# Kernel optimization log

Measured on AMD Instinct MI355X. Metric: run time of the kernel, lower is better.

## Reference

```python
import jax, jax.numpy as jnp
import numpy as np

B, C, H, W, NH = 8, 256, 32, 32, 4  # batch, channels, height, width, heads


def groupnorm(x, w, b, eps=1e-5):
    # GroupNorm with 1 group: normalize over (C,H,W) per sample
    mu = x.mean(axis=(1, 2, 3), keepdims=True)
    var = x.var(axis=(1, 2, 3), keepdims=True)
    xn = (x - mu) * jax.lax.rsqrt(var + eps)
    return xn * w[None, :, None, None] + b[None, :, None, None]


def setup_inputs() -> dict:
    key = jax.random.key(0)
    ks = jax.random.split(key, 6)
    C4 = 4 * C
    s = lambda k, shape, scale: jax.random.normal(k, shape, jnp.float32) * scale
    return {
        "x": jax.random.normal(ks[0], (B, C, H, W), jnp.float32),
        "qkv_w": s(ks[1], (3 * C, C), 0.05),   # 1x1 conv, no bias
        "uh_w": s(ks[2], (C, C), 0.05),
        "uh_b": jnp.zeros((C,), jnp.float32),
        "n1_w": jnp.ones((C,), jnp.float32),
        "n1_b": jnp.zeros((C,), jnp.float32),
        "n2_w": jnp.ones((C,), jnp.float32),
        "n2_b": jnp.zeros((C,), jnp.float32),
        "f1_w": s(ks[3], (C4, C), 0.05),
        "f1_b": jnp.zeros((C4,), jnp.float32),
        "f2_w": s(ks[4], (C, C4), 0.05),
        "f2_b": jnp.zeros((C,), jnp.float32),
        # torch inits these to 0; use nonzero values so both branches contribute
        "gamma_attn": jnp.array(0.5, jnp.float32),
        "gamma_ffn": jnp.array(0.5, jnp.float32),
    }


def reference(x, qkv_w, uh_w, uh_b, n1_w, n1_b, n2_w, n2_b,
              f1_w, f1_b, f2_w, f2_b, gamma_attn, gamma_ffn):
    Bx, Cx, Hx, Wx = x.shape
    N = Hx * Wx
    dk = Cx // NH
    # --- attention branch (eval mode: DropPath is identity) ---
    xn = groupnorm(x, n1_w, n1_b).reshape(Bx, Cx, N)
    qkv = jnp.einsum('oc,bcn->bon', qkv_w, xn)          # 1x1 conv == channel matmul
    q, k, v = [t.reshape(Bx, NH, dk, N) for t in jnp.split(qkv, 3, axis=1)]
    scores = jnp.einsum('bhdi,bhdj->bhij', q, k) / np.float32(np.sqrt(dk))
    attn = jax.nn.softmax(scores, axis=-1)               # [B,H,N,N]
    out = jnp.einsum('bhij,bhdj->bhdi', attn, v).reshape(Bx, Cx, N)
    uh = jnp.einsum('oc,bcn->bon', uh_w, out) + uh_b[None, :, None]
    x2 = x + gamma_attn * uh.reshape(Bx, Cx, Hx, Wx)
    # --- FFN branch ---
    h = groupnorm(x2, n2_w, n2_b).reshape(Bx, Cx, N)
    h = jax.nn.silu(jnp.einsum('oc,bcn->bon', f1_w, h) + f1_b[None, :, None])
    h = jnp.einsum('oc,bcn->bon', f2_w, h) + f2_b[None, :, None]
    return x2 + gamma_ffn * h.reshape(Bx, Cx, Hx, Wx)
```

## Files before the change

### kernel.cpp

```cpp
#include <hip/hip_runtime.h>
#include <math.h>

#define Bsz 8
#define Cch 256
#define Nsp 1024
#define NHd 4
#define QS  0.18033688011112042f

using bf16x8  = __attribute__((ext_vector_type(8))) short;
using f32x4   = __attribute__((ext_vector_type(4))) float;
using ushort8 = __attribute__((ext_vector_type(8))) unsigned short;
#define MFMA(a,b,c) __builtin_amdgcn_mfma_f32_16x16x32_bf16(a,b,c,0,0,0)

__device__ inline unsigned short f2bf(float f) {
    unsigned int u = __float_as_uint(f);
    u = u + 0x7fffu + ((u >> 16) & 1u);
    return (unsigned short)(u >> 16);
}
__device__ inline float bf2f(unsigned short u) {
    return __uint_as_float((unsigned int)u << 16);
}
__device__ inline unsigned int cvtpk(float lo, float hi) {
    unsigned int r;
    asm("v_cvt_pk_bf16_f32 %0, %1, %2" : "=v"(r) : "v"(lo), "v"(hi));
    return r;
}

__global__ __launch_bounds__(256) void wconv_gn(const float* __restrict__ a, const float* __restrict__ b,
                                                const float* __restrict__ c, const float* __restrict__ d,
                                                unsigned short* __restrict__ o,
                                                const float* __restrict__ x,
                                                float* __restrict__ part) {
    if (blockIdx.x < 3072) {
        size_t i = (size_t)blockIdx.x * 256 + threadIdx.x;
        float v;
        if (i < 196608) v = a[i];
        else if (i < 262144) v = b[i - 196608];
        else if (i < 524288) v = c[i - 262144];
        else v = d[i - 524288];
        o[i] = f2bf(v);
        return;
    }
    int blk = blockIdx.x - 3072;
    int bb = blk >> 6;
    const float* xb = x + (size_t)bb * (Cch * Nsp) + (size_t)(blk & 63) * 4096;
    int t = threadIdx.x;
    float s = 0.f, s2 = 0.f;
    for (int i = t; i < 4096; i += 256) { float v = xb[i]; s += v; s2 += v * v; }
    __shared__ float sh[256], sh2[256];
    sh[t] = s; sh2[t] = s2; __syncthreads();
    for (int off = 128; off; off >>= 1) {
        if (t < off) { sh[t] += sh[t + off]; sh2[t] += sh2[t + off]; }
        __syncthreads();
    }
    if (t == 0) { part[blk * 2] = sh[0]; part[blk * 2 + 1] = sh2[0]; }
}

template<int K, int KL, int NFRAG>
__global__ __launch_bounds__(256, 4) void gemm_lds(
        const unsigned short* __restrict__ W,
        const unsigned short* __restrict__ Xcl,
        int epi, int act, int xmode,
        unsigned short* __restrict__ ocl, int Ocl, int ocol0,
        unsigned short* __restrict__ orm,
        float* __restrict__ pf, const float* __restrict__ res,
        unsigned short* __restrict__ x2cl,
        const float* __restrict__ gamma, const float* __restrict__ bias,
        float* __restrict__ part,
        const float* __restrict__ gnpart,
        const float* __restrict__ gnw, const float* __restrict__ gnb) {
    static_assert(KL == 256 && K == 256, "single-round K only");
    constexpr int NTILE = NFRAG * 16;
    constexpr int CPR = KL / 8;
    constexpr int TOTCH = NTILE * CPR;
    int b = blockIdx.z, nb = blockIdx.x, ob = blockIdx.y;
    int t = threadIdx.x, w = t >> 6, l = t & 63, lg = l >> 4, lm = l & 15;
    __shared__ unsigned short Xs[NTILE * KL];
    __shared__ float sgn[2];
    const unsigned short* Xb = Xcl + ((size_t)b * Nsp + nb * NTILE) * K;
    int o_base = ob * 256 + w * 64;
    const unsigned short* Wp = W + (size_t)(o_base + lm) * K + 8 * lg;
    int m8 = lm & 7;

    bf16x8 wA0, wA1, wA2, wA3, wB0, wB1, wB2, wB3, wC0, wC1, wC2, wC3;
    #define WL(d0, d1, d2, d3, ks_) do {                                   \
        d0 = *(const bf16x8*)(Wp + (size_t)(0)      + (ks_) * 32);         \
        d1 = *(const bf16x8*)(Wp + (size_t)16 * K   + (ks_) * 32);         \
        d2 = *(const bf16x8*)(Wp + (size_t)32 * K   + (ks_) * 32);         \
        d3 = *(const bf16x8*)(Wp + (size_t)48 * K   + (ks_) * 32);         \
    } while (0)
    WL(wA0, wA1, wA2, wA3, 0);
    WL(wB0, wB1, wB2, wB3, 1);

    if (xmode == 0) {
        #pragma unroll
        for (int i = 0; i < TOTCH / 256; i++) {
            int c = i * 256 + t;
            int n = c / CPR, s = c % CPR;
            int gc = s ^ (n & 7);
            *(bf16x8*)&Xs[c * 8] = *(const bf16x8*)(Xb + (size_t)n * K + gc * 8);
        }
    } else if (xmode == 1) {
        if (t < 64) {
            float s = gnpart[(b * 64 + t) * 2], s2 = gnpart[(b * 64 + t) * 2 + 1];
            for (int m = 1; m < 64; m <<= 1) { s += __shfl_xor(s, m); s2 += __shfl_xor(s2, m); }
            if (t == 0) {
                float inv_n = 1.f / (Cch * Nsp);
                float mu = s * inv_n;
                float var = s2 * inv_n - mu * mu;
                sgn[0] = mu; sgn[1] = rsqrtf(var + 1e-5f);
            }
        }
        __syncthreads();
        float mu = sgn[0], rs = sgn[1];
        #pragma unroll
        for (int i = 0; i < TOTCH / 256; i++) {
            int c = i * 256 + t;
            int n = c / CPR, s = c % CPR;
            int gc = s ^ (n & 7);
            ushort8 xv = *(const ushort8*)(Xb + (size_t)n * K + gc * 8);
            f32x4 w0 = *(const f32x4*)(gnw + gc * 8);
            f32x4 w1 = *(const f32x4*)(gnw + gc * 8 + 4);
            f32x4 b0 = *(const f32x4*)(gnb + gc * 8);
            f32x4 b1 = *(const f32x4*)(gnb + gc * 8 + 4);
            ushort8 rr;
            #pragma unroll
            for (int j = 0; j < 4; j++) {
                rr[j]     = f2bf((bf2f(xv[j])     - mu) * rs * w0[j] + b0[j]);
                rr[4 + j] = f2bf((bf2f(xv[4 + j]) - mu) * rs * w1[j] + b1[j]);
            }
            *(ushort8*)&Xs[c * 8] = rr;
        }
    } else if (xmode == 2) {
        const size_t SPO = (size_t)Bsz * Nsp * Cch;
        #pragma unroll
        for (int i = 0; i < TOTCH / 256; i++) {
            int c = i * 256 + t;
            int n = c / CPR, s = c % CPR;
            int gc = s ^ (n & 7);
            const unsigned short* p0 = Xb + (size_t)n * K + gc * 8;
            int h = gc >> 3;
            int gn = nb * NTILE + n;
            float a0[8] = {};
            float lsum = 0.f;
            #pragma unroll
            for (int sp = 0; sp < 4; sp++) {
                ushort8 ov = *(const ushort8*)(p0 + (size_t)sp * SPO);
                #pragma unroll
                for (int j = 0; j < 8; j++) a0[j] += bf2f(ov[j]);
                lsum += gnpart[(((size_t)sp * Bsz + b) * NHd + h) * Nsp + gn];
            }
            float inv = 1.f / lsum;
            ushort8 rr;
            #pragma unroll
            for (int j = 0; j < 8; j++) rr[j] = f2bf(a0[j] * inv);
            *(ushort8*)&Xs[c * 8] = rr;
        }
    } else {
        if (t < 64) {
            float s = gnpart[(b * 64 + t) * 2], s2 = gnpart[(b * 64 + t) * 2 + 1];
            for (int m = 1; m < 64; m <<= 1) { s += __shfl_xor(s, m); s2 += __shfl_xor(s2, m); }
            if (t == 0) {
                float inv_n = 1.f / (Cch * Nsp);
                float mu = s * inv_n;
                float var = s2 * inv_n - mu * mu;
                sgn[0] = mu; sgn[1] = rsqrtf(var + 1e-5f);
            }
        }
        __syncthreads();
        float mu = sgn[0], rs = sgn[1];
        int n = t & 31;
        #pragma unroll
        for (int i = 0; i < 4; i++) {
            int G = i * 8 + (t >> 5);
            const float* xr = res + ((size_t)b * Cch + G * 8) * Nsp + (size_t)nb * NTILE + n;
            ushort8 rr;
            #pragma unroll
            for (int j = 0; j < 8; j++) {
                float val = xr[(size_t)j * Nsp];
                rr[j] = f2bf((val - mu) * rs * gnw[G * 8 + j] + gnb[G * 8 + j]);
            }
            int slot = G ^ (n & 7);
            *(ushort8*)&Xs[(n * 32 + slot) * 8] = rr;
        }
    }
    __syncthreads();

    f32x4 acc[4][NFRAG] = {};
    #define KS(w0_, w1_, w2_, w3_, ks_) do {                               \
        _Pragma("unroll")                                                  \
        for (int nf = 0; nf < NFRAG; nf++) {                               \
            int slot = ((ks_) * 4 + lg) ^ m8;                              \
            bf16x8 xf = *(const bf16x8*)&Xs[((nf * 16 + lm) * CPR + slot) * 8]; \
            acc[0][nf] = MFMA(w0_, xf, acc[0][nf]);                        \
            acc[1][nf] = MFMA(w1_, xf, acc[1][nf]);                        \
            acc[2][nf] = MFMA(w2_, xf, acc[2][nf]);                        \
            acc[3][nf] = MFMA(w3_, xf, acc[3][nf]);                        \
        }                                                                  \
    } while (0)
    WL(wC0, wC1, wC2, wC3, 2); KS(wA0, wA1, wA2, wA3, 0);
    WL(wA0, wA1, wA2, wA3, 3); KS(wB0, wB1, wB2, wB3, 1);
    WL(wB0, wB1, wB2, wB3, 4); KS(wC0, wC1, wC2, wC3, 2);
    WL(wC0, wC1, wC2, wC3, 5); KS(wA0, wA1, wA2, wA3, 3);
    WL(wA0, wA1, wA2, wA3, 6); KS(wB0, wB1, wB2, wB3, 4);
    WL(wB0, wB1, wB2, wB3, 7); KS(wC0, wC1, wC2, wC3, 5);
    KS(wA0, wA1, wA2, wA3, 6);
    KS(wB0, wB1, wB2, wB3, 7);
    #undef WL
    #undef KS

    if (epi == 0) {
        if (act == 3 && o_base >= 512) {
            #pragma unroll
            for (int nf = 0; nf < NFRAG; nf++) {
                int n = nb * NTILE + nf * 16 + lm;
                #pragma unroll
                for (int q = 0; q < 4; q++)
                    #pragma unroll
                    for (int r = 0; r < 4; r++) {
                        int o = o_base + q * 16 + 4 * lg + r - 512;
                        orm[((size_t)b * Cch + o) * Nsp + n] = f2bf(acc[q][nf][r]);
                    }
            }
        } else {
            float sc = (act == 3 && o_base < 256) ? QS : 1.f;
            #pragma unroll
            for (int nf = 0; nf < NFRAG; nf++) {
                int n = nb * NTILE + nf * 16 + lm;
                unsigned short* dst = ocl + ((size_t)b * Nsp + n) * Ocl + ocol0 + o_base + 4 * lg;
                #pragma unroll
                for (int q = 0; q < 4; q++) {
                    unsigned long long pk = 0;
                    #pragma unroll
                    for (int r = 0; r < 4; r++) {
                        int o = o_base + q * 16 + 4 * lg + r;
                        float v = acc[q][nf][r];
                        if (bias) v += bias[o];
                        if (act == 1) v = v / (1.f + __expf(-v));
                        else v *= sc;
                        pk |= (unsigned long long)f2bf(v) << (16 * r);
                    }
                    *(unsigned long long*)(dst + q * 16) = pk;
                }
            }
        }
    } else {
        float g = gamma[0];
        float ps = 0.f, ps2 = 0.f;
        #pragma unroll
        for (int nf = 0; nf < NFRAG; nf++) {
            int n = nb * NTILE + nf * 16 + lm;
            unsigned short* cdst = x2cl + ((size_t)b * Nsp + n) * Cch + o_base + 4 * lg;
            #pragma unroll
            for (int q = 0; q < 4; q++) {
                unsigned long long pk = 0;
                #pragma unroll
                for (int r = 0; r < 4; r++) {
                    int o = o_base + q * 16 + 4 * lg + r;
                    float v = acc[q][nf][r];
                    if (bias) v += bias[o];
                    size_t idx = ((size_t)b * Cch + o) * Nsp + n;
                    float ov = res[idx] + g * v;
                    pf[idx] = ov;
                    ps += ov; ps2 += ov * ov;
                    pk |= (unsigned long long)f2bf(ov) << (16 * r);
                }
                *(unsigned long long*)(cdst + q * 16) = pk;
            }
        }
        float* rsh  = (float*)&Xs[0];
        float* rsh2 = rsh + 256;
        __syncthreads();
        rsh[t] = ps; rsh2[t] = ps2; __syncthreads();
        for (int off = 128; off; off >>= 1) {
            if (t < off) { rsh[t] += rsh[t + off]; rsh2[t] += rsh2[t + off]; }
            __syncthreads();
        }
        if (t == 0) {
            int slot = b * gridDim.x + nb;
            part[slot * 2] = rsh[0]; part[slot * 2 + 1] = rsh2[0];
        }
    }
}

__global__ __launch_bounds__(512, 2) void ffn_fused(
        const unsigned short* __restrict__ Wf1,
        const unsigned short* __restrict__ Wf2,
        const unsigned short* __restrict__ x2cl,
        const float* __restrict__ gnpart,
        const float* __restrict__ gnw, const float* __restrict__ gnb,
        const float* __restrict__ f1b, const float* __restrict__ f2b,
        const float* __restrict__ gamma,
        const float* __restrict__ x2, float* __restrict__ out) {
    int b = blockIdx.z, nb = blockIdx.x;
    int t = threadIdx.x, w = t >> 6, l = t & 63, lg = l >> 4, lm = l & 15;
    int wq = w >> 2, wr = w & 3;
    __shared__ unsigned short Xs[32 * 256];
    __shared__ unsigned short H[4][32 * 256];
    __shared__ float sgn[2];
    const unsigned short* Xb = x2cl + ((size_t)b * Nsp + nb * 32) * 256;
    int m8 = lm & 7;

    bf16x8 wA0, wA1, wA2, wA3, wB0, wB1, wB2, wB3, wC0, wC1, wC2, wC3;
    const unsigned short* Wp;
    #define WL1(d0, d1, d2, d3, ks_) do {                                  \
        d0 = *(const bf16x8*)(Wp + (ks_) * 32);                            \
        d1 = *(const bf16x8*)(Wp + (size_t)16 * 256 + (ks_) * 32);         \
        d2 = *(const bf16x8*)(Wp + (size_t)32 * 256 + (ks_) * 32);         \
        d3 = *(const bf16x8*)(Wp + (size_t)48 * 256 + (ks_) * 32);         \
    } while (0)

    if (t < 64) {
        float s = gnpart[(b * 64 + t) * 2], s2 = gnpart[(b * 64 + t) * 2 + 1];
        for (int m = 1; m < 64; m <<= 1) { s += __shfl_xor(s, m); s2 += __shfl_xor(s2, m); }
        if (t == 0) {
            float inv_n = 1.f / (Cch * Nsp);
            float mu = s * inv_n;
            float var = s2 * inv_n - mu * mu;
            sgn[0] = mu; sgn[1] = rsqrtf(var + 1e-5f);
        }
    }
    Wp = Wf1 + (size_t)(wq * 256 + wr * 64 + lm) * 256 + 8 * lg;
    WL1(wA0, wA1, wA2, wA3, 0);
    WL1(wB0, wB1, wB2, wB3, 1);
    __syncthreads();
    {
        float mu = sgn[0], rs = sgn[1];
        #pragma unroll
        for (int i = 0; i < 2; i++) {
            int c = i * 512 + t;
            int n = c >> 5, s = c & 31;
            int gc = s ^ (n & 7);
            ushort8 xv = *(const ushort8*)(Xb + (size_t)n * 256 + gc * 8);
            f32x4 w0 = *(const f32x4*)(gnw + gc * 8);
            f32x4 w1 = *(const f32x4*)(gnw + gc * 8 + 4);
            f32x4 b0 = *(const f32x4*)(gnb + gc * 8);
            f32x4 b1 = *(const f32x4*)(gnb + gc * 8 + 4);
            ushort8 rr;
            #pragma unroll
            for (int j = 0; j < 4; j++) {
                rr[j]     = f2bf((bf2f(xv[j])     - mu) * rs * w0[j] + b0[j]);
                rr[4 + j] = f2bf((bf2f(xv[4 + j]) - mu) * rs * w1[j] + b1[j]);
            }
            *(ushort8*)&Xs[c * 8] = rr;
        }
    }
    __syncthreads();

    f32x4 acc[4][2];
    #define KS1(w0_, w1_, w2_, w3_, ks_) do {                              \
        _Pragma("unroll")                                                  \
        for (int nf = 0; nf < 2; nf++) {                                   \
            int slot = ((ks_) * 4 + lg) ^ m8;                              \
            bf16x8 xf = *(const bf16x8*)&Xs[((nf * 16 + lm) * 32 + slot) * 8]; \
            acc[0][nf] = MFMA(w0_, xf, acc[0][nf]);                        \
            acc[1][nf] = MFMA(w1_, xf, acc[1][nf]);                        \
            acc[2][nf] = MFMA(w2_, xf, acc[2][nf]);                        \
            acc[3][nf] = MFMA(w3_, xf, acc[3][nf]);                        \
        }                                                                  \
    } while (0)
    #define F1CHAIN() do {                                                 \
        WL1(wC0, wC1, wC2, wC3, 2); KS1(wA0, wA1, wA2, wA3, 0);            \
        WL1(wA0, wA1, wA2, wA3, 3); KS1(wB0, wB1, wB2, wB3, 1);            \
        WL1(wB0, wB1, wB2, wB3, 4); KS1(wC0, wC1, wC2, wC3, 2);            \
        WL1(wC0, wC1, wC2, wC3, 5); KS1(wA0, wA1, wA2, wA3, 3);            \
        WL1(wA0, wA1, wA2, wA3, 6); KS1(wB0, wB1, wB2, wB3, 4);            \
        WL1(wB0, wB1, wB2, wB3, 7); KS1(wC0, wC1, wC2, wC3, 5);            \
        KS1(wA0, wA1, wA2, wA3, 6);                                        \
        KS1(wB0, wB1, wB2, wB3, 7);                                        \
    } while (0)
    #define F1EPI(p_) do {                                                 \
        int hb = (p_) * 2 + wq;                                            \
        _Pragma("unroll")                                                  \
        for (int nf = 0; nf < 2; nf++) {                                   \
            int n = nf * 16 + lm;                                          \
            _Pragma("unroll")                                              \
            for (int q = 0; q < 4; q++) {                                  \
                unsigned long long pk = 0;                                 \
                _Pragma("unroll")                                          \
                for (int r = 0; r < 4; r++) {                              \
                    int oin = wr * 64 + q * 16 + 4 * lg + r;               \
                    float v = acc[q][nf][r] + f1b[(p_) * 512 + wq * 256 + oin]; \
                    v = v / (1.f + __expf(-v));                            \
                    pk |= (unsigned long long)f2bf(v) << (16 * r);         \
                }                                                          \
                int G = wr * 8 + q * 2 + (lg >> 1);                        \
                int slot = G ^ (n & 7);                                    \
                *(unsigned long long*)&H[hb][(n * 32 + slot) * 8 + 4 * (lg & 1)] = pk; \
            }                                                              \
        }                                                                  \
    } while (0)

    #pragma unroll
    for (int q = 0; q < 4; q++)
        #pragma unroll
        for (int nf = 0; nf < 2; nf++) acc[q][nf] = (f32x4){0.f, 0.f, 0.f, 0.f};
    F1CHAIN();
    Wp = Wf1 + (size_t)(512 + wq * 256 + wr * 64 + lm) * 256 + 8 * lg;
    WL1(wA0, wA1, wA2, wA3, 0);
    WL1(wB0, wB1, wB2, wB3, 1);
    F1EPI(0);
    #pragma unroll
    for (int q = 0; q < 4; q++)
        #pragma unroll
        for (int nf = 0; nf < 2; nf++) acc[q][nf] = (f32x4){0.f, 0.f, 0.f, 0.f};
    F1CHAIN();
    #undef WL1
    #undef KS1
    #undef F1CHAIN

    const unsigned short* Wp2 = Wf2 + (size_t)(w * 32 + lm) * 1024 + 8 * lg;
    bf16x8 u0, u1, v0, v1, z0, z1;
    #define WL2(d0, d1, ks_) do {                                          \
        d0 = *(const bf16x8*)(Wp2 + (ks_) * 32);                           \
        d1 = *(const bf16x8*)(Wp2 + (size_t)16 * 1024 + (ks_) * 32);       \
    } while (0)
    WL2(u0, u1, 0);
    WL2(v0, v1, 1);
    F1EPI(1);
    #undef F1EPI
    __syncthreads();

    f32x4 ac2[2][2] = {};
    #define KS2(e0, e1, g_) do {                                           \
        int slot = (((g_) & 7) * 4 + lg) ^ m8;                             \
        const unsigned short* Hp = H[(g_) >> 3];                           \
        _Pragma("unroll")                                                  \
        for (int nf = 0; nf < 2; nf++) {                                   \
            bf16x8 xf = *(const bf16x8*)&Hp[((nf * 16 + lm) * 32 + slot) * 8]; \
            ac2[0][nf] = MFMA(e0, xf, ac2[0][nf]);                         \
            ac2[1][nf] = MFMA(e1, xf, ac2[1][nf]);                         \
        }                                                                  \
    } while (0)
    WL2(z0, z1, 2);  KS2(u0, u1, 0);
    WL2(u0, u1, 3);  KS2(v0, v1, 1);
    WL2(v0, v1, 4);  KS2(z0, z1, 2);
    WL2(z0, z1, 5);  KS2(u0, u1, 3);
    WL2(u0, u1, 6);  KS2(v0, v1, 4);
    WL2(v0, v1, 7);  KS2(z0, z1, 5);
    WL2(z0, z1, 8);  KS2(u0, u1, 6);
    WL2(u0, u1, 9);  KS2(v0, v1, 7);
    WL2(v0, v1, 10); KS2(z0, z1, 8);
    WL2(z0, z1, 11); KS2(u0, u1, 9);
    WL2(u0, u1, 12); KS2(v0, v1, 10);
    WL2(v0, v1, 13); KS2(z0, z1, 11);
    WL2(z0, z1, 14); KS2(u0, u1, 12);
    WL2(u0, u1, 15); KS2(v0, v1, 13);
    WL2(v0, v1, 16); KS2(z0, z1, 14);
    WL2(z0, z1, 17); KS2(u0, u1, 15);
    WL2(u0, u1, 18); KS2(v0, v1, 16);
    WL2(v0, v1, 19); KS2(z0, z1, 17);
    WL2(z0, z1, 20); KS2(u0, u1, 18);
    WL2(u0, u1, 21); KS2(v0, v1, 19);
    WL2(v0, v1, 22); KS2(z0, z1, 20);
    WL2(z0, z1, 23); KS2(u0, u1, 21);
    WL2(u0, u1, 24); KS2(v0, v1, 22);
    WL2(v0, v1, 25); KS2(z0, z1, 23);
    WL2(z0, z1, 26); KS2(u0, u1, 24);
    WL2(u0, u1, 27); KS2(v0, v1, 25);
    WL2(v0, v1, 28); KS2(z0, z1, 26);
    WL2(z0, z1, 29); KS2(u0, u1, 27);
    WL2(u0, u1, 30); KS2(v0, v1, 28);
    WL2(v0, v1, 31); KS2(z0, z1, 29);
    KS2(u0, u1, 30);
    KS2(v0, v1, 31);
    #undef WL2
    #undef KS2

    float gm = gamma[0];
    #pragma unroll
    for (int nf = 0; nf < 2; nf++) {
        int n = nb * 32 + nf * 16 + lm;
        #pragma unroll
        for (int ch = 0; ch < 2; ch++) {
            #pragma unroll
            for (int r = 0; r < 4; r++) {
                int o = w * 32 + ch * 16 + 4 * lg + r;
                size_t idx = ((size_t)b * Cch + o) * Nsp + n;
                out[idx] = x2[idx] + gm * (ac2[ch][nf][r] + f2b[o]);
            }
        }
    }
}

__global__ __launch_bounds__(256) void attn_mfma8(const unsigned short* __restrict__ qk,
                                                  const unsigned short* __restrict__ v,
                                                  unsigned short* __restrict__ Opart,
                                                  float* __restrict__ lpart) {
    int L = blockIdx.x;
    int xcd = L & 7, jj = L >> 3;
    int g = xcd * 4 + (jj >> 5);
    int m = jj & 31;
    int h = g & 3, b = g >> 2;
    int ib = m & 7, sp = m >> 3;
    int t = threadIdx.x, w = t >> 6, l = t & 63, lg = l >> 4, lm = l & 15;
    __shared__ unsigned short KVs[2][4096];
    __shared__ unsigned short P[4][2][32][36];
    int i0 = ib * 128 + w * 32;
    int j0 = sp * 256;
    const unsigned short* qb = qk + ((size_t)b * Nsp + i0 + lm) * 512 + h * 64 + 8 * lg;
    bf16x8 qf00 = *(const bf16x8*)(qb);
    bf16x8 qf01 = *(const bf16x8*)(qb + 32);
    bf16x8 qf10 = *(const bf16x8*)(qb + 16 * 512);
    bf16x8 qf11 = *(const bf16x8*)(qb + 16 * 512 + 32);

    const unsigned short *gs0, *gs1;
    int lo0, lo1;
    size_t gstep;
    if (t < 128) {
        int c = 2 * t;
        int r = c >> 3, s = c & 7, swr = r & 7;
        const unsigned short* rowp = qk + ((size_t)b * Nsp + j0 + r) * 512 + 256 + h * 64;
        gs0 = rowp + ((s ^ swr) * 8);
        gs1 = rowp + (((s + 1) ^ swr) * 8);
        lo0 = c * 8; lo1 = lo0 + 8;
        gstep = (size_t)32 * 512;
    } else {
        int c = 2 * (t - 128);
        int d = c >> 2, s = c & 3, swd = d & 3;
        const unsigned short* rowp = v + ((size_t)b * Cch + h * 64 + d) * Nsp + j0;
        gs0 = rowp + ((s ^ swd) * 8);
        gs1 = rowp + (((s + 1) ^ swd) * 8);
        lo0 = 2048 + c * 8; lo1 = lo0 + 8;
        gstep = 32;
    }
    int cA = (lg ^ (lm & 7)) * 8;
    int cB = ((4 + lg) ^ (lm & 7)) * 8;
    int cV = (lg ^ (lm & 3)) * 8;

    f32x4 O00 = {}, O01 = {}, O02 = {}, O03 = {};
    f32x4 O10 = {}, O11 = {}, O12 = {}, O13 = {};
    float ls0 = 0.f, ls1 = 0.f;
    bf16x8 sg0, sg1;

    #define ISSUE(tile) do { sg0 = *(const bf16x8*)(gs0 + (size_t)(tile) * gstep); \
                             sg1 = *(const bf16x8*)(gs1 + (size_t)(tile) * gstep); } while (0)
    #define WRITE(bu) do { *(bf16x8*)&KVs[bu][lo0] = sg0; \
                           *(bf16x8*)&KVs[bu][lo1] = sg1; } while (0)
    #define QKC8(bu, pb) do {                                                     \
        const unsigned short* Ka = KVs[bu] + lm * 64;                             \
        const unsigned short* Kc = KVs[bu] + (16 + lm) * 64;                      \
        bf16x8 k00 = *(const bf16x8*)(Ka + cA);                                   \
        bf16x8 k01 = *(const bf16x8*)(Ka + cB);                                   \
        bf16x8 k10 = *(const bf16x8*)(Kc + cA);                                   \
        bf16x8 k11 = *(const bf16x8*)(Kc + cB);                                   \
        f32x4 s00 = {}, s01 = {}, s10 = {}, s11 = {};                             \
        s00 = MFMA(k00, qf00, s00); s00 = MFMA(k01, qf01, s00);                   \
        s01 = MFMA(k00, qf10, s01); s01 = MFMA(k01, qf11, s01);                   \
        s10 = MFMA(k10, qf00, s10); s10 = MFMA(k11, qf01, s10);                   \
        s11 = MFMA(k10, qf10, s11); s11 = MFMA(k11, qf11, s11);                   \
        float p0, p1, p2, p3; uint2 pk;                                           \
        p0 = exp2f(s00[0]); p1 = exp2f(s00[1]); p2 = exp2f(s00[2]); p3 = exp2f(s00[3]); \
        ls0 += (p0 + p1) + (p2 + p3);                                             \
        pk.x = cvtpk(p0, p1); pk.y = cvtpk(p2, p3);                               \
        *(uint2*)&P[w][pb][lm][4 * lg] = pk;                                      \
        p0 = exp2f(s01[0]); p1 = exp2f(s01[1]); p2 = exp2f(s01[2]); p3 = exp2f(s01[3]); \
        ls1 += (p0 + p1) + (p2 + p3);                                             \
        pk.x = cvtpk(p0, p1); pk.y = cvtpk(p2, p3);                               \
        *(uint2*)&P[w][pb][16 + lm][4 * lg] = pk;                                 \
        p0 = exp2f(s10[0]); p1 = exp2f(s10[1]); p2 = exp2f(s10[2]); p3 = exp2f(s10[3]); \
        ls0 += (p0 + p1) + (p2 + p3);                                             \
        pk.x = cvtpk(p0, p1); pk.y = cvtpk(p2, p3);                               \
        *(uint2*)&P[w][pb][lm][16 + 4 * lg] = pk;                                 \
        p0 = exp2f(s11[0]); p1 = exp2f(s11[1]); p2 = exp2f(s11[2]); p3 = exp2f(s11[3]); \
        ls1 += (p0 + p1) + (p2 + p3);                                             \
        pk.x = cvtpk(p0, p1); pk.y = cvtpk(p2, p3);                               \
        *(uint2*)&P[w][pb][16 + lm][16 + 4 * lg] = pk;                            \
    } while (0)
    #define PVC8(bu, pb) do {                                                     \
        bf16x8 pa0 = *(const bf16x8*)&P[w][pb][lm][8 * lg];                       \
        bf16x8 pa1 = *(const bf16x8*)&P[w][pb][16 + lm][8 * lg];                  \
        const unsigned short* Vl = KVs[bu] + 2048;                                \
        bf16x8 v0 = *(const bf16x8*)(Vl + lm * 32 + cV);                          \
        bf16x8 v1 = *(const bf16x8*)(Vl + (16 + lm) * 32 + cV);                   \
        bf16x8 v2 = *(const bf16x8*)(Vl + (32 + lm) * 32 + cV);                   \
        bf16x8 v3 = *(const bf16x8*)(Vl + (48 + lm) * 32 + cV);                   \
        O00 = MFMA(v0, pa0, O00); O10 = MFMA(v0, pa1, O10);                       \
        O01 = MFMA(v1, pa0, O01); O11 = MFMA(v1, pa1, O11);                       \
        O02 = MFMA(v2, pa0, O02); O12 = MFMA(v2, pa1, O12);                       \
        O03 = MFMA(v3, pa0, O03); O13 = MFMA(v3, pa1, O13);                       \
    } while (0)

    ISSUE(0); WRITE(0); __syncthreads();
    ISSUE(1);
    QKC8(0, 0);
    __syncthreads();
    WRITE(1);
    __syncthreads();
    #pragma unroll
    for (int tt = 1; tt < 8; tt++) {
        if (tt < 7) ISSUE(tt + 1);
        QKC8(tt & 1, tt & 1);
        PVC8((tt - 1) & 1, (tt - 1) & 1);
        __syncthreads();
        if (tt < 7) WRITE((tt + 1) & 1);
        __syncthreads();
    }
    PVC8(1, 1);
    #undef ISSUE
    #undef WRITE
    #undef QKC8
    #undef PVC8

    ls0 += __shfl_xor(ls0, 16); ls0 += __shfl_xor(ls0, 32);
    ls1 += __shfl_xor(ls1, 16); ls1 += __shfl_xor(ls1, 32);
    if (lg == 0) {
        float* lp = lpart + (((size_t)sp * Bsz + b) * NHd + h) * Nsp + i0 + lm;
        lp[0] = ls0;
        lp[16] = ls1;
    }
    unsigned short* ob0 = Opart + (((size_t)sp * Bsz + b) * Nsp + i0 + lm) * Cch + h * 64 + 4 * lg;
    unsigned short* ob1 = ob0 + (size_t)16 * Cch;
    uint2 pk;
    #define STO(dt, Oa, Ob_) \
        pk.x = cvtpk(Oa[0], Oa[1]); pk.y = cvtpk(Oa[2], Oa[3]); \
        *(uint2*)(ob0 + dt * 16) = pk; \
        pk.x = cvtpk(Ob_[0], Ob_[1]); pk.y = cvtpk(Ob_[2], Ob_[3]); \
        *(uint2*)(ob1 + dt * 16) = pk;
    STO(0, O00, O10) STO(1, O01, O11) STO(2, O02, O12) STO(3, O03, O13)
    #undef STO
}

extern "C" void kernel_launch(void* const* d_in, const int* in_sizes, int n_in,
                              void* d_out, int out_size, void* d_ws, size_t ws_size,
                              hipStream_t stream) {
    const float* x      = (const float*)d_in[0];
    const float* qkv_w  = (const float*)d_in[1];
    const float* uh_w   = (const float*)d_in[2];
    const float* uh_b   = (const float*)d_in[3];
    const float* n1_w   = (const float*)d_in[4];
    const float* n1_b   = (const float*)d_in[5];
    const float* n2_w   = (const float*)d_in[6];
    const float* n2_b   = (const float*)d_in[7];
    const float* f1_w   = (const float*)d_in[8];
    const float* f1_b   = (const float*)d_in[9];
    const float* f2_w   = (const float*)d_in[10];
    const float* f2_b   = (const float*)d_in[11];
    const float* g_attn = (const float*)d_in[12];
    const float* g_ffn  = (const float*)d_in[13];
    float* out = (float*)d_out;
    char* ws = (char*)d_ws;

    float*          part1   = (float*)(ws + 1024);
    float*          part2   = (float*)(ws + 5120);
    unsigned short* wbf     = (unsigned short*)(ws + 16384);
    float*          lpart   = (float*)(ws + 2097152);
    unsigned short* qk_cl   = (unsigned short*)(ws + 6291456);
    unsigned short* vbuf    = (unsigned short*)(ws + 14680064);
    unsigned short* x2cl    = (unsigned short*)(ws + 14680064);
    unsigned short* Opart   = (unsigned short*)(ws + 23068672);
    float*          x2      = (float*)(ws + 50331648);

    unsigned short* wbf_qkv = wbf;
    unsigned short* wbf_uh  = wbf + 196608;
    unsigned short* wbf_f1  = wbf + 262144;
    unsigned short* wbf_f2  = wbf + 524288;

    wconv_gn<<<3584, 256, 0, stream>>>(qkv_w, uh_w, f1_w, f2_w, wbf, x, part1);

    gemm_lds<256, 256, 2><<<dim3(32, 3, Bsz), 256, 0, stream>>>(wbf_qkv,
        (const unsigned short*)x, 0, 3, 3,
        qk_cl, 512, 0, vbuf, nullptr, x, nullptr, nullptr, nullptr, nullptr,
        part1, n1_w, n1_b);
    attn_mfma8<<<1024, 256, 0, stream>>>(qk_cl, vbuf, Opart, lpart);
    gemm_lds<256, 256, 1><<<dim3(64, 1, Bsz), 256, 0, stream>>>(wbf_uh, Opart, 2, 0, 2,
        nullptr, 0, 0, nullptr, x2, x, x2cl, g_attn, uh_b, part2,
        lpart, nullptr, nullptr);

    ffn_fused<<<dim3(32, 1, Bsz), 512, 0, stream>>>(wbf_f1, wbf_f2, x2cl,
        part2, n2_w, n2_b, f1_b, f2_b, g_ffn, x2, out);
}
```

Baseline: 106.0 us.

## Double FFN block to 1024 threads and halve per-wave work

ffn_fused now launches 1024 threads per block instead of 512. Each wave computes a single 64-row slice of the first FFN GEMM in one pass instead of two sequential passes. In the second GEMM each wave produces 16 output channels instead of 32, with a shorter rotating register buffer for the weights. The grid is only 256 blocks, so the goal is more waves per CU to hide latency and shorten the serial chain. The cost is the tighter register budget implied by __launch_bounds__(1024, 4), which could force spills.

```diff
diff --git a/kernel.cpp b/kernel.cpp
--- a/kernel.cpp
+++ b/kernel.cpp
@@ -283,7 +283,7 @@
     }
 }
 
-__global__ __launch_bounds__(512, 2) void ffn_fused(
+__global__ __launch_bounds__(1024, 4) void ffn_fused(
         const unsigned short* __restrict__ Wf1,
         const unsigned short* __restrict__ Wf2,
         const unsigned short* __restrict__ x2cl,
@@ -294,7 +294,6 @@
         const float* __restrict__ x2, float* __restrict__ out) {
     int b = blockIdx.z, nb = blockIdx.x;
     int t = threadIdx.x, w = t >> 6, l = t & 63, lg = l >> 4, lm = l & 15;
-    int wq = w >> 2, wr = w & 3;
     __shared__ unsigned short Xs[32 * 256];
     __shared__ unsigned short H[4][32 * 256];
     __shared__ float sgn[2];
@@ -302,7 +301,7 @@
     int m8 = lm & 7;
 
     bf16x8 wA0, wA1, wA2, wA3, wB0, wB1, wB2, wB3, wC0, wC1, wC2, wC3;
-    const unsigned short* Wp;
+    const unsigned short* Wp = Wf1 + (size_t)(w * 64 + lm) * 256 + 8 * lg;
     #define WL1(d0, d1, d2, d3, ks_) do {                                  \
         d0 = *(const bf16x8*)(Wp + (ks_) * 32);                            \
         d1 = *(const bf16x8*)(Wp + (size_t)16 * 256 + (ks_) * 32);         \
@@ -320,34 +319,34 @@
             sgn[0] = mu; sgn[1] = rsqrtf(var + 1e-5f);
         }
     }
-    Wp = Wf1 + (size_t)(wq * 256 + wr * 64 + lm) * 256 + 8 * lg;
     WL1(wA0, wA1, wA2, wA3, 0);
     WL1(wB0, wB1, wB2, wB3, 1);
     __syncthreads();
     {
         float mu = sgn[0], rs = sgn[1];
-        #pragma unroll
-        for (int i = 0; i < 2; i++) {
-            int c = i * 512 + t;
-            int n = c >> 5, s = c & 31;
-            int gc = s ^ (n & 7);
-            ushort8 xv = *(const ushort8*)(Xb + (size_t)n * 256 + gc * 8);
-            f32x4 w0 = *(const f32x4*)(gnw + gc * 8);
-            f32x4 w1 = *(const f32x4*)(gnw + gc * 8 + 4);
-            f32x4 b0 = *(const f32x4*)(gnb + gc * 8);
-            f32x4 b1 = *(const f32x4*)(gnb + gc * 8 + 4);
-            ushort8 rr;
-            #pragma unroll
-            for (int j = 0; j < 4; j++) {
-                rr[j]     = f2bf((bf2f(xv[j])     - mu) * rs * w0[j] + b0[j]);
-                rr[4 + j] = f2bf((bf2f(xv[4 + j]) - mu) * rs * w1[j] + b1[j]);
-            }
-            *(ushort8*)&Xs[c * 8] = rr;
-        }
+        int c = t;
+        int n = c >> 5, s = c & 31;
+        int gc = s ^ (n & 7);
+        ushort8 xv = *(const ushort8*)(Xb + (size_t)n * 256 + gc * 8);
+        f32x4 w0 = *(const f32x4*)(gnw + gc * 8);
+        f32x4 w1 = *(const f32x4*)(gnw + gc * 8 + 4);
+        f32x4 b0 = *(const f32x4*)(gnb + gc * 8);
+        f32x4 b1 = *(const f32x4*)(gnb + gc * 8 + 4);
+        ushort8 rr;
+        #pragma unroll
+        for (int j = 0; j < 4; j++) {
+            rr[j]     = f2bf((bf2f(xv[j])     - mu) * rs * w0[j] + b0[j]);
+            rr[4 + j] = f2bf((bf2f(xv[4 + j]) - mu) * rs * w1[j] + b1[j]);
+        }
+        *(ushort8*)&Xs[c * 8] = rr;
     }
     __syncthreads();
 
     f32x4 acc[4][2];
+    #pragma unroll
+    for (int q = 0; q < 4; q++)
+        #pragma unroll
+        for (int nf = 0; nf < 2; nf++) acc[q][nf] = (f32x4){0.f, 0.f, 0.f, 0.f};
     #define KS1(w0_, w1_, w2_, w3_, ks_) do {                              \
         _Pragma("unroll")                                                  \
         for (int nf = 0; nf < 2; nf++) {                                   \
@@ -359,111 +358,87 @@
             acc[3][nf] = MFMA(w3_, xf, acc[3][nf]);                        \
         }                                                                  \
     } while (0)
-    #define F1CHAIN() do {                                                 \
-        WL1(wC0, wC1, wC2, wC3, 2); KS1(wA0, wA1, wA2, wA3, 0);            \
-        WL1(wA0, wA1, wA2, wA3, 3); KS1(wB0, wB1, wB2, wB3, 1);            \
-        WL1(wB0, wB1, wB2, wB3, 4); KS1(wC0, wC1, wC2, wC3, 2);            \
-        WL1(wC0, wC1, wC2, wC3, 5); KS1(wA0, wA1, wA2, wA3, 3);            \
-        WL1(wA0, wA1, wA2, wA3, 6); KS1(wB0, wB1, wB2, wB3, 4);            \
-        WL1(wB0, wB1, wB2, wB3, 7); KS1(wC0, wC1, wC2, wC3, 5);            \
-        KS1(wA0, wA1, wA2, wA3, 6);                                        \
-        KS1(wB0, wB1, wB2, wB3, 7);                                        \
-    } while (0)
-    #define F1EPI(p_) do {                                                 \
-        int hb = (p_) * 2 + wq;                                            \
-        _Pragma("unroll")                                                  \
-        for (int nf = 0; nf < 2; nf++) {                                   \
-            int n = nf * 16 + lm;                                          \
-            _Pragma("unroll")                                              \
-            for (int q = 0; q < 4; q++) {                                  \
-                unsigned long long pk = 0;                                 \
-                _Pragma("unroll")                                          \
-                for (int r = 0; r < 4; r++) {                              \
-                    int oin = wr * 64 + q * 16 + 4 * lg + r;               \
-                    float v = acc[q][nf][r] + f1b[(p_) * 512 + wq * 256 + oin]; \
-                    v = v / (1.f + __expf(-v));                            \
-                    pk |= (unsigned long long)f2bf(v) << (16 * r);         \
-                }                                                          \
-                int G = wr * 8 + q * 2 + (lg >> 1);                        \
-                int slot = G ^ (n & 7);                                    \
-                *(unsigned long long*)&H[hb][(n * 32 + slot) * 8 + 4 * (lg & 1)] = pk; \
-            }                                                              \
-        }                                                                  \
-    } while (0)
-
-    #pragma unroll
-    for (int q = 0; q < 4; q++)
-        #pragma unroll
-        for (int nf = 0; nf < 2; nf++) acc[q][nf] = (f32x4){0.f, 0.f, 0.f, 0.f};
-    F1CHAIN();
-    Wp = Wf1 + (size_t)(512 + wq * 256 + wr * 64 + lm) * 256 + 8 * lg;
-    WL1(wA0, wA1, wA2, wA3, 0);
-    WL1(wB0, wB1, wB2, wB3, 1);
-    F1EPI(0);
-    #pragma unroll
-    for (int q = 0; q < 4; q++)
-        #pragma unroll
-        for (int nf = 0; nf < 2; nf++) acc[q][nf] = (f32x4){0.f, 0.f, 0.f, 0.f};
-    F1CHAIN();
+    WL1(wC0, wC1, wC2, wC3, 2); KS1(wA0, wA1, wA2, wA3, 0);
+    WL1(wA0, wA1, wA2, wA3, 3); KS1(wB0, wB1, wB2, wB3, 1);
+    WL1(wB0, wB1, wB2, wB3, 4); KS1(wC0, wC1, wC2, wC3, 2);
+    WL1(wC0, wC1, wC2, wC3, 5); KS1(wA0, wA1, wA2, wA3, 3);
+    WL1(wA0, wA1, wA2, wA3, 6); KS1(wB0, wB1, wB2, wB3, 4);
+    WL1(wB0, wB1, wB2, wB3, 7); KS1(wC0, wC1, wC2, wC3, 5);
+    KS1(wA0, wA1, wA2, wA3, 6);
+    KS1(wB0, wB1, wB2, wB3, 7);
     #undef WL1
     #undef KS1
-    #undef F1CHAIN
-
-    const unsigned short* Wp2 = Wf2 + (size_t)(w * 32 + lm) * 1024 + 8 * lg;
-    bf16x8 u0, u1, v0, v1, z0, z1;
-    #define WL2(d0, d1, ks_) do {                                          \
-        d0 = *(const bf16x8*)(Wp2 + (ks_) * 32);                           \
-        d1 = *(const bf16x8*)(Wp2 + (size_t)16 * 1024 + (ks_) * 32);       \
-    } while (0)
-    WL2(u0, u1, 0);
-    WL2(v0, v1, 1);
-    F1EPI(1);
-    #undef F1EPI
+
+    const unsigned short* Wp2 = Wf2 + (size_t)(w * 16 + lm) * 1024 + 8 * lg;
+    bf16x8 fa, fb, fc, fd, fe, ff;
+    #define WL2(d0, ks_) d0 = *(const bf16x8*)(Wp2 + (ks_) * 32)
+    WL2(fa, 0); WL2(fb, 1); WL2(fc, 2); WL2(fd, 3);
+
+    {
+        int hb = w >> 2;
+        #pragma unroll
+        for (int nf = 0; nf < 2; nf++) {
+            int n = nf * 16 + lm;
+            #pragma unroll
+            for (int q = 0; q < 4; q++) {
+                unsigned long long pk = 0;
+                #pragma unroll
+                for (int r = 0; r < 4; r++) {
+                    int o1 = w * 64 + q * 16 + 4 * lg + r;
+                    float v = acc[q][nf][r] + f1b[o1];
+                    v = v / (1.f + __expf(-v));
+                    pk |= (unsigned long long)f2bf(v) << (16 * r);
+                }
+                int G = (w & 3) * 8 + q * 2 + (lg >> 1);
+                int slot = G ^ (n & 7);
+                *(unsigned long long*)&H[hb][(n * 32 + slot) * 8 + 4 * (lg & 1)] = pk;
+            }
+        }
+    }
     __syncthreads();
 
-    f32x4 ac2[2][2] = {};
-    #define KS2(e0, e1, g_) do {                                           \
+    f32x4 ac2[2] = {};
+    #define KS2(e0, g_) do {                                               \
         int slot = (((g_) & 7) * 4 + lg) ^ m8;                             \
         const unsigned short* Hp = H[(g_) >> 3];                           \
         _Pragma("unroll")                                                  \
         for (int nf = 0; nf < 2; nf++) {                                   \
             bf16x8 xf = *(const bf16x8*)&Hp[((nf * 16 + lm) * 32 + slot) * 8]; \
-            ac2[0][nf] = MFMA(e0, xf, ac2[0][nf]);                         \
-            ac2[1][nf] = MFMA(e1, xf, ac2[1][nf]);                         \
+            ac2[nf] = MFMA(e0, xf, ac2[nf]);                               \
         }                                                                  \
     } while (0)
-    WL2(z0, z1, 2);  KS2(u0, u1, 0);
-    WL2(u0, u1, 3);  KS2(v0, v1, 1);
-    WL2(v0, v1, 4);  KS2(z0, z1, 2);
-    WL2(z0, z1, 5);  KS2(u0, u1, 3);
-    WL2(u0, u1, 6);  KS2(v0, v1, 4);
-    WL2(v0, v1, 7);  KS2(z0, z1, 5);
-    WL2(z0, z1, 8);  KS2(u0, u1, 6);
-    WL2(u0, u1, 9);  KS2(v0, v1, 7);
-    WL2(v0, v1, 10); KS2(z0, z1, 8);
-    WL2(z0, z1, 11); KS2(u0, u1, 9);
-    WL2(u0, u1, 12); KS2(v0, v1, 10);
-    WL2(v0, v1, 13); KS2(z0, z1, 11);
-    WL2(z0, z1, 14); KS2(u0, u1, 12);
-    WL2(u0, u1, 15); KS2(v0, v1, 13);
-    WL2(v0, v1, 16); KS2(z0, z1, 14);
-    WL2(z0, z1, 17); KS2(u0, u1, 15);
-    WL2(u0, u1, 18); KS2(v0, v1, 16);
-    WL2(v0, v1, 19); KS2(z0, z1, 17);
-    WL2(z0, z1, 20); KS2(u0, u1, 18);
-    WL2(u0, u1, 21); KS2(v0, v1, 19);
-    WL2(v0, v1, 22); KS2(z0, z1, 20);
-    WL2(z0, z1, 23); KS2(u0, u1, 21);
-    WL2(u0, u1, 24); KS2(v0, v1, 22);
-    WL2(v0, v1, 25); KS2(z0, z1, 23);
-    WL2(z0, z1, 26); KS2(u0, u1, 24);
-    WL2(u0, u1, 27); KS2(v0, v1, 25);
-    WL2(v0, v1, 28); KS2(z0, z1, 26);
-    WL2(z0, z1, 29); KS2(u0, u1, 27);
-    WL2(u0, u1, 30); KS2(v0, v1, 28);
-    WL2(v0, v1, 31); KS2(z0, z1, 29);
-    KS2(u0, u1, 30);
-    KS2(v0, v1, 31);
+    WL2(fe, 4);  KS2(fa, 0);
+    WL2(ff, 5);  KS2(fb, 1);
+    WL2(fa, 6);  KS2(fc, 2);
+    WL2(fb, 7);  KS2(fd, 3);
+    WL2(fc, 8);  KS2(fe, 4);
+    WL2(fd, 9);  KS2(ff, 5);
+    WL2(fe, 10); KS2(fa, 6);
+    WL2(ff, 11); KS2(fb, 7);
+    WL2(fa, 12); KS2(fc, 8);
+    WL2(fb, 13); KS2(fd, 9);
+    WL2(fc, 14); KS2(fe, 10);
+    WL2(fd, 15); KS2(ff, 11);
+    WL2(fe, 16); KS2(fa, 12);
+    WL2(ff, 17); KS2(fb, 13);
+    WL2(fa, 18); KS2(fc, 14);
+    WL2(fb, 19); KS2(fd, 15);
+    WL2(fc, 20); KS2(fe, 16);
+    WL2(fd, 21); KS2(ff, 17);
+    WL2(fe, 22); KS2(fa, 18);
+    WL2(ff, 23); KS2(fb, 19);
+    WL2(fa, 24); KS2(fc, 20);
+    WL2(fb, 25); KS2(fd, 21);
+    WL2(fc, 26); KS2(fe, 22);
+    WL2(fd, 27); KS2(ff, 23);
+    WL2(fe, 28); KS2(fa, 24);
+    WL2(ff, 29); KS2(fb, 25);
+    WL2(fa, 30); KS2(fc, 26);
+    WL2(fb, 31); KS2(fd, 27);
+    KS2(fe, 28);
+    KS2(ff, 29);
+    KS2(fa, 30);
+    KS2(fb, 31);
     #undef WL2
     #undef KS2
 
@@ -472,13 +447,10 @@
     for (int nf = 0; nf < 2; nf++) {
         int n = nb * 32 + nf * 16 + lm;
         #pragma unroll
-        for (int ch = 0; ch < 2; ch++) {
-            #pragma unroll
-            for (int r = 0; r < 4; r++) {
-                int o = w * 32 + ch * 16 + 4 * lg + r;
-                size_t idx = ((size_t)b * Cch + o) * Nsp + n;
-                out[idx] = x2[idx] + gm * (ac2[ch][nf][r] + f2b[o]);
-            }
+        for (int r = 0; r < 4; r++) {
+            int o = w * 16 + 4 * lg + r;
+            size_t idx = ((size_t)b * Cch + o) * Nsp + n;
+            out[idx] = x2[idx] + gm * (ac2[nf][r] + f2b[o]);
         }
     }
 }
@@ -667,6 +639,6 @@
         nullptr, 0, 0, nullptr, x2, x, x2cl, g_attn, uh_b, part2,
         lpart, nullptr, nullptr);
 
-    ffn_fused<<<dim3(32, 1, Bsz), 512, 0, stream>>>(wbf_f1, wbf_f2, x2cl,
+    ffn_fused<<<dim3(32, 1, Bsz), 1024, 0, stream>>>(wbf_f1, wbf_f2, x2cl,
         part2, n2_w, n2_b, f1_b, f2_b, g_ffn, x2, out);
 }
```

New measurement: 106.0 us. About the same (-0.0%).
